# Performance work log

Measured on AMD Instinct MI355X. Metric: run time of the kernel, lower is better.

Reference implementation:

```python
import jax, jax.numpy as jnp
import numpy as np

MIN_NORM = 1e-15
BALL_EPS = 4e-3  # float32 boundary eps used by the PoincareBall manifold


def _norm(x):
    return jnp.maximum(jnp.linalg.norm(x, axis=-1, keepdims=True), MIN_NORM)


def _artanh(x):
    # clamp like torch Artanh autograd fn (1e-7 margin)
    return jnp.arctanh(jnp.clip(x, -1.0 + 1e-7, 1.0 - 1e-7))


def proj(x, c):
    n = _norm(x)
    maxnorm = (1.0 - BALL_EPS) / jnp.sqrt(c)
    return jnp.where(n > maxnorm, x / n * maxnorm, x)


def expmap0(u, c):
    sc = jnp.sqrt(c)
    n = _norm(u)
    return jnp.tanh(sc * n) * u / (sc * n)


def logmap0(p, c):
    sc = jnp.sqrt(c)
    n = _norm(p)
    return _artanh(sc * n) * p / (sc * n)


def mobius_add(x, y, c):
    x2 = jnp.sum(x * x, axis=-1, keepdims=True)
    y2 = jnp.sum(y * y, axis=-1, keepdims=True)
    xy = jnp.sum(x * y, axis=-1, keepdims=True)
    num = (1.0 + 2.0 * c * xy + c * y2) * x + (1.0 - c * x2) * y
    denom = 1.0 + 2.0 * c * xy + c * c * x2 * y2
    return num / jnp.maximum(denom, MIN_NORM)


def mobius_matvec(m, x, c):
    sc = jnp.sqrt(c)
    xn = _norm(x)
    mx = x @ m.T  # [N, out]
    mxn = _norm(mx)
    res = jnp.tanh(mxn / xn * _artanh(sc * xn)) * mx / (mxn * sc)
    is_zero = jnp.all(mx == 0, axis=-1, keepdims=True)
    return jnp.where(is_zero, jnp.zeros_like(res), res)


def setup_inputs() -> dict:
    key = jax.random.key(0)
    N, D_IN, D_OUT, E = 100000, 128, 128, 1600000
    k1, k2, k3, k4, k5 = jax.random.split(key, 5)
    # points inside the Poincare ball (||x|| ~ 0.34 < 1)
    x = 0.03 * jax.random.normal(k1, (N, D_IN), dtype=jnp.float32)
    # xavier_uniform with gain sqrt(2)
    limit = np.sqrt(2.0) * np.sqrt(6.0 / (D_IN + D_OUT))
    weight = jax.random.uniform(k2, (D_OUT, D_IN), minval=-limit, maxval=limit, dtype=jnp.float32)
    bias = jnp.zeros((D_OUT,), dtype=jnp.float32)
    edge_index = jax.random.randint(k3, (2, E), 0, N, dtype=jnp.int64)
    edge_weight = jax.random.uniform(k4, (E,), dtype=jnp.float32) / 16.0
    return {"x": x, "weight": weight, "bias": bias,
            "edge_index": edge_index, "edge_weight": edge_weight,
            "num_nodes": N}


def reference(x, weight, bias, edge_index, edge_weight, num_nodes):
    c_in = 1.0
    c_out = 1.0
    # --- OriginHypLinear (dropout=0 / eval) ---
    mv = proj(mobius_matvec(weight, x, c_in), c_in)
    hyp_bias = proj(expmap0(bias[None, :], c_in), c_in)  # proj_tan0 is identity
    h = proj(mobius_add(mv, hyp_bias, c_in), c_in)
    # --- OriginHypAgg: logmap0 -> spmm -> expmap0 ---
    xt = logmap0(h, c_in)
    dst, src = edge_index[0], edge_index[1]
    support = jax.ops.segment_sum(edge_weight[:, None] * xt[src], dst,
                                  num_segments=num_nodes)
    h = proj(expmap0(support, c_in), c_in)
    # --- OriginHypAct: relu in tangent space ---
    xt = jax.nn.relu(logmap0(h, c_in))  # proj_tan0 identity
    return proj(expmap0(xt, c_out), c_out)
```

## Files before the change

kernel.cpp:

```cpp
#include <hip/hip_runtime.h>
#include <math.h>

#define D 128
#define MAXNORM 0.996f
#define MINNORM 1e-15f
#define ATCLAMP (1.0f - 1e-7f)

#define CHUNK 2048
#define BSH   7
#define MAXNB 1024
#define SCAP2 5120
#define CAP   4096
#define TCAP  (1 << 20)

typedef unsigned int   u32;
typedef unsigned short u16;

typedef __attribute__((ext_vector_type(8))) _Float16 f16x8;
typedef __attribute__((ext_vector_type(2))) __fp16   h2raw;
typedef __attribute__((ext_vector_type(4))) float f32x4;

__device__ __forceinline__ float wsum(float v) {
#pragma unroll
  for (int m = 32; m; m >>= 1) v += __shfl_xor(v, m);
  return v;
}
__device__ __forceinline__ float rsum16(float v) {
#pragma unroll
  for (int m = 1; m <= 8; m <<= 1) v += __shfl_xor(v, m);
  return v;
}

__device__ __forceinline__ float frcp(float x) { return __builtin_amdgcn_rcpf(x); }

__device__ __forceinline__ float fast_artanh(float x) {
  x = fminf(x, ATCLAMP);
  return 0.5f * __logf((1.0f + x) * frcp(1.0f - x));
}
__device__ __forceinline__ float fast_tanh(float z) {
  float t = __expf(-2.0f * z);
  return (1.0f - t) * frcp(1.0f + t);
}

__device__ __forceinline__ float bflo(u32 u) { return __uint_as_float(u << 16); }
__device__ __forceinline__ float bfhi(u32 u) { return __uint_as_float(u & 0xffff0000u); }
__device__ __forceinline__ float bf2f(u16 h) { return __uint_as_float(((u32)h) << 16); }

union H2U { h2raw h; u32 u; };
__device__ __forceinline__ u32 pkh(float a, float b) {
  H2U c; c.h = __builtin_amdgcn_cvt_pkrtz(a, b); return c.u;
}
union U2H { u32 u; _Float16 h[2]; };
union U4H8 { uint4 u; f16x8 h; };
__device__ __forceinline__ f16x8 as_h8(uint4 v) { U4H8 c; c.u = v; return c.h; }
__device__ __forceinline__ u16 f2h(float f) {
  _Float16 h = (_Float16)f; return *(u16*)&h;
}

__device__ __forceinline__ bool detect_bf16(const u32* p) {
  float lo = fabsf(bflo(p[threadIdx.x & 63]));
  return (bool)__all(lo < 1.0f);
}
__device__ __forceinline__ bool detect_i64(const int* p) {
  return (bool)__all(p[2 * (threadIdx.x & 63) + 1] == 0);
}

template<bool BF>
__device__ __forceinline__ void k1_body(const void* xv, const void* Wv,
                                        const void* bv, u16* xt, int N,
                                        uint4* Wh) {
  const int tid  = threadIdx.x;
  const int lane = tid & 63;
  const int wid  = tid >> 6;
  const int qg   = lane >> 4;
  const int lc   = lane & 15;

  for (int slot = tid; slot < 2048; slot += 256) {
    const int l = slot & 63, frag = slot >> 6;
    const int t = frag >> 2, ks = frag & 3;
    const int j  = (l & 15) + 16 * t;
    const int k0 = 32 * ks + 8 * (l >> 4);
    float f[8];
    if (BF) {
      uint4 v = ((const uint4*)Wv)[j * 16 + (k0 >> 3)];
      f[0] = bflo(v.x); f[1] = bfhi(v.x); f[2] = bflo(v.y); f[3] = bfhi(v.y);
      f[4] = bflo(v.z); f[5] = bfhi(v.z); f[6] = bflo(v.w); f[7] = bfhi(v.w);
    } else {
      const float* Wf = (const float*)Wv;
      float4 f0 = *(const float4*)(Wf + (size_t)j * D + k0);
      float4 f1 = *(const float4*)(Wf + (size_t)j * D + k0 + 4);
      f[0]=f0.x; f[1]=f0.y; f[2]=f0.z; f[3]=f0.w;
      f[4]=f1.x; f[5]=f1.y; f[6]=f1.z; f[7]=f1.w;
    }
    Wh[slot] = make_uint4(pkh(f[0],f[1]), pkh(f[2],f[3]),
                          pkh(f[4],f[5]), pkh(f[6],f[7]));
  }

  float bfr[8];
  float nb2 = 0.f;
#pragma unroll
  for (int t = 0; t < 8; ++t) {
    float v = BF ? bf2f(((const u16*)bv)[lc + 16 * t])
                 : ((const float*)bv)[lc + 16 * t];
    bfr[t] = v; nb2 += v * v;
  }
  nb2 = rsum16(nb2);
  float y2;
  {
    float nb = fmaxf(sqrtf(nb2), MINNORM);
    float s  = fast_tanh(nb) * frcp(nb);
    float n1 = s * nb;
    if (n1 > MAXNORM) s *= MAXNORM * frcp(n1);
#pragma unroll
    for (int t = 0; t < 8; ++t) bfr[t] *= s;
    y2 = s * s * nb2;
  }
  const bool bias_zero = (y2 == 0.0f);

  __syncthreads();

  const int T = (N + 15) >> 4;
  const int tile = blockIdx.x * 4 + wid;
  if (tile >= T) return;
  {
    const int rbase = tile * 16;
    int rowA = rbase + lc; if (rowA >= N) rowA = N - 1;
    uint4 Ah[4];
    float xn2 = 0.f;
#pragma unroll
    for (int ks = 0; ks < 4; ++ks) {
      float f[8];
      if (BF) {
        uint4 v = ((const uint4*)((const u16*)xv + (size_t)rowA * D))[4 * ks + qg];
        f[0]=bflo(v.x); f[1]=bfhi(v.x); f[2]=bflo(v.y); f[3]=bfhi(v.y);
        f[4]=bflo(v.z); f[5]=bfhi(v.z); f[6]=bflo(v.w); f[7]=bfhi(v.w);
      } else {
        const float4* xr = (const float4*)((const float*)xv + (size_t)rowA * D);
        float4 f0 = xr[8 * ks + 2 * qg], f1 = xr[8 * ks + 2 * qg + 1];
        f[0]=f0.x; f[1]=f0.y; f[2]=f0.z; f[3]=f0.w;
        f[4]=f1.x; f[5]=f1.y; f[6]=f1.z; f[7]=f1.w;
      }
#pragma unroll
      for (int i = 0; i < 8; ++i) xn2 += f[i] * f[i];
      Ah[ks] = make_uint4(pkh(f[0],f[1]), pkh(f[2],f[3]),
                          pkh(f[4],f[5]), pkh(f[6],f[7]));
    }
    xn2 += __shfl_xor(xn2, 16);
    xn2 += __shfl_xor(xn2, 32);

    f32x4 acc[8];
    const f32x4 zero = {0.f, 0.f, 0.f, 0.f};
#pragma unroll
    for (int t = 0; t < 8; ++t) acc[t] = zero;
#pragma unroll
    for (int ks = 0; ks < 4; ++ks) {
      f16x8 a = as_h8(Ah[ks]);
#pragma unroll
      for (int t = 0; t < 8; ++t) {
        f16x8 bh = as_h8(Wh[(t * 4 + ks) * 64 + lane]);
        acc[t] = __builtin_amdgcn_mfma_f32_16x16x32_f16(a, bh, acc[t], 0, 0, 0);
      }
    }

#pragma unroll
    for (int q = 0; q < 4; ++q) {
      const int row_off = qg * 4 + q;
      const int row = rbase + row_off;
      float xnq = fmaxf(sqrtf(__shfl(xn2, row_off)), MINNORM);
      float s2 = 0.f;
#pragma unroll
      for (int t = 0; t < 8; ++t) { float v = acc[t][q]; s2 += v * v; }
      s2 = rsum16(s2);
      float mxn = fmaxf(sqrtf(s2), MINNORM);
      float r = fast_tanh(mxn * frcp(xnq) * fast_artanh(xnq)) * frcp(mxn);
      float pn = r * mxn;
      if (pn > MAXNORM) { r *= MAXNORM * frcp(pn); pn = MAXNORM; }
      float h[8];
      float hn;
      if (bias_zero) {
#pragma unroll
        for (int t = 0; t < 8; ++t) h[t] = r * acc[t][q];
        hn = pn;
      } else {
        float xy = 0.f;
#pragma unroll
        for (int t = 0; t < 8; ++t) { h[t] = r * acc[t][q]; xy += h[t] * bfr[t]; }
        xy = rsum16(xy);
        float x2 = pn * pn;
        float ca = 1.f + 2.f * xy + y2;
        float cb = 1.f - x2;
        float id = frcp(fmaxf(1.f + 2.f * xy + x2 * y2, MINNORM));
        float s3 = 0.f;
#pragma unroll
        for (int t = 0; t < 8; ++t) { h[t] = (ca * h[t] + cb * bfr[t]) * id; s3 += h[t] * h[t]; }
        hn = fmaxf(sqrtf(rsum16(s3)), MINNORM);
      }
      float ps = (hn > MAXNORM) ? (MAXNORM * frcp(hn)) : 1.f;
      float np = fmaxf(hn * ps, MINNORM);
      float tsc = fast_artanh(np) * frcp(np) * ps;
      if (row < N) {
        uint4 pk;
        pk.x = (u32)f2h(tsc * h[0]) | ((u32)f2h(tsc * h[1]) << 16);
        pk.y = (u32)f2h(tsc * h[2]) | ((u32)f2h(tsc * h[3]) << 16);
        pk.z = (u32)f2h(tsc * h[4]) | ((u32)f2h(tsc * h[5]) << 16);
        pk.w = (u32)f2h(tsc * h[6]) | ((u32)f2h(tsc * h[7]) << 16);
        *(uint4*)(xt + (size_t)row * D + lc * 8) = pk;
      }
    }
  }
}

__device__ __forceinline__ void ksA_body(
    const int* ei, const void* ew, uint2* ebuck, u16* soffs,
    int E, int N, int nb, int chunk, uint4* lds) {
  uint2* recs = (uint2*)lds;
  int*   hist = (int*)(lds + 1024);
  int*   sArr = hist + MAXNB;
  int*   psum = sArr + MAXNB + 1;
  const bool i64 = detect_i64(ei);
  const bool bf  = detect_bf16((const u32*)ew);
  const int tid   = threadIdx.x;
  const int cbase = chunk * CHUNK;

  for (int i = tid; i < MAXNB; i += 256) hist[i] = 0;
  __syncthreads();

  int bkt[8], rank[8]; u32 px[8], wb[8]; bool val[8];
#pragma unroll
  for (int r = 0; r < 8; ++r) {
    const int e = cbase + r * 256 + tid;
    val[r] = false;
    if (e < E) {
      int dst, src;
      if (i64) {
        dst = (int)((const uint2*)ei)[(size_t)e].x;
        src = (int)((const uint2*)ei)[(size_t)E + e].x;
      } else {
        dst = ei[e]; src = ei[(size_t)E + e];
      }
      if ((unsigned)dst < (unsigned)N && (unsigned)src < (unsigned)N) {
        val[r] = true;
        bkt[r] = dst >> BSH;
        px[r]  = (u32)src | ((u32)(dst & ((1 << BSH) - 1)) << 17);
        float w;
        if (bf) w = bf2f(((const u16*)ew)[e]); else w = ((const float*)ew)[e];
        wb[r] = __float_as_uint(w);
        rank[r] = atomicAdd(&hist[bkt[r]], 1);
      }
    }
  }
  __syncthreads();

  const int g0 = tid * 4;
  int loc[4], ts = 0;
#pragma unroll
  for (int i = 0; i < 4; ++i) { loc[i] = ts; ts += hist[g0 + i]; }
  psum[tid] = ts; __syncthreads();
#pragma unroll
  for (int off = 1; off < 256; off <<= 1) {
    int t = (tid >= off) ? psum[tid - off] : 0;
    __syncthreads();
    psum[tid] += t;
    __syncthreads();
  }
  const int excl = psum[tid] - ts;
#pragma unroll
  for (int i = 0; i < 4; ++i) sArr[g0 + i] = excl + loc[i];
  if (tid == 255) sArr[MAXNB] = psum[255];
  __syncthreads();

#pragma unroll
  for (int r = 0; r < 8; ++r) if (val[r])
    recs[sArr[bkt[r]] + rank[r]] = make_uint2(px[r], wb[r]);
  __syncthreads();

  const int vcnt = sArr[MAXNB];
  for (int i = tid; i < vcnt; i += 256) ebuck[(size_t)cbase + i] = recs[i];
  u16* so = soffs + (size_t)chunk * (nb + 1);
  for (int b = tid; b <= nb; b += 256) so[b] = (u16)sArr[b];
}

extern "C" __global__ __launch_bounds__(256)
void OriginHyperbolicGraphConvolution_38628935860614_kernel(
    const void* x, const void* W, const void* b, u16* xt,
    const int* ei, const void* ew, uint2* ebuck, u16* soffs, int* tailcur,
    int N, int E, int nb, int nk1) {
  __shared__ uint4 Wh[2048];
  if (blockIdx.x == 0 && threadIdx.x == 0) *tailcur = 0;
  if ((int)blockIdx.x < nk1) {
    if (detect_bf16((const u32*)x)) k1_body<true >(x, W, b, xt, N, Wh);
    else                            k1_body<false>(x, W, b, xt, N, Wh);
  } else {
    ksA_body(ei, ew, ebuck, soffs, E, N, nb, (int)blockIdx.x - nk1, Wh);
  }
}

extern "C" __global__ __launch_bounds__(256) void ks3(
    const uint2* ebuck, const u16* soffs, uint2* esrt, uint2* offs2,
    int* tailcur, int N, int nb, int nchunks) {
  __shared__ uint2 stage[SCAP2];
  __shared__ int red[256];
  __shared__ int hist[128], sc[128], cur[128];
  __shared__ int lcur;
  __shared__ u32 sbase;
  const int tid = threadIdx.x;
  const int b = blockIdx.x;
  const int node0 = b << BSH;

  int myc = 0;
  for (int c = tid; c < nchunks; c += 256) {
    const u16* so = soffs + (size_t)c * (nb + 1) + b;
    myc += (int)so[1] - (int)so[0];
  }
  red[tid] = myc;
  if (tid < 128) hist[tid] = 0;
  if (tid == 0) lcur = 0;
  __syncthreads();
#pragma unroll
  for (int off = 128; off; off >>= 1) {
    if (tid < off) red[tid] += red[tid + off];
    __syncthreads();
  }
  const int cnt = red[0];
  if (tid == 0)
    sbase = (cnt <= CAP) ? (u32)((size_t)b * CAP)
                         : (u32)((size_t)nb * CAP + (u32)atomicAdd(tailcur, cnt));
  __syncthreads();
  const u32 base = sbase;

  const bool fit = (cnt <= SCAP2);
  if (fit) {
    for (int c = tid; c < nchunks; c += 256) {
      const u16* so = soffs + (size_t)c * (nb + 1) + b;
      const int a = so[0], e = so[1];
      if (e > a) {
        const int sb = atomicAdd(&lcur, e - a);
        for (int j = a; j < e; ++j) {
          const uint2 r = ebuck[(size_t)c * CHUNK + j];
          stage[sb + (j - a)] = r;
          atomicAdd(&hist[(r.x >> 17) & 127], 1);
        }
      }
    }
  } else {
    for (int c = tid; c < nchunks; c += 256) {
      const u16* so = soffs + (size_t)c * (nb + 1) + b;
      for (int j = so[0]; j < so[1]; ++j)
        atomicAdd(&hist[(ebuck[(size_t)c * CHUNK + j].x >> 17) & 127], 1);
    }
  }
  __syncthreads();

  int v = 0;
  if (tid < 128) { v = hist[tid]; sc[tid] = v; }
  __syncthreads();
#pragma unroll
  for (int off = 1; off < 128; off <<= 1) {
    int t = (tid < 128 && tid >= off) ? sc[tid - off] : 0;
    __syncthreads();
    if (tid < 128) sc[tid] += t;
    __syncthreads();
  }
  if (tid < 128) {
    const int st = sc[tid] - v;
    cur[tid] = st;
    const int node = node0 + tid;
    if (node < N) offs2[node] = make_uint2(base + (u32)st, (u32)v);
  }
  __syncthreads();

  if (fit) {
    for (int i = tid; i < cnt; i += 256) {
      const uint2 r = stage[i];
      const int d = atomicAdd(&cur[(r.x >> 17) & 127], 1);
      esrt[(size_t)base + d] = make_uint2(r.x & 0x1FFFFu, r.y);
    }
  } else {
    for (int c = tid; c < nchunks; c += 256) {
      const u16* so = soffs + (size_t)c * (nb + 1) + b;
      for (int j = so[0]; j < so[1]; ++j) {
        const uint2 r = ebuck[(size_t)c * CHUNK + j];
        const int d = atomicAdd(&cur[(r.x >> 17) & 127], 1);
        esrt[(size_t)base + d] = make_uint2(r.x & 0x1FFFFu, r.y);
      }
    }
  }
}

extern "C" __global__ __launch_bounds__(256) void kagg(
    const uint2* offs2, const uint2* esrt, const u16* xt,
    void* out, const void* xdet, int N) {
  const bool bf = detect_bf16((const u32*)xdet);
  const int lane = threadIdx.x & 63;
  const int node = blockIdx.x * 4 + (threadIdx.x >> 6);
  if (node >= N) return;
  const uint2 oo = offs2[node];
  const int s0  = __builtin_amdgcn_readfirstlane((int)oo.x);
  const int cnt = __builtin_amdgcn_readfirstlane((int)oo.y);
  const uint2* ep = esrt + s0;
  const u32* xtw = (const u32*)xt;
  float a0 = 0.f, a1 = 0.f;
  int i = 0;
  for (; i + 16 <= cnt; i += 16) {
    uint2 e[16]; u32 u[16];
#pragma unroll
    for (int k = 0; k < 16; ++k) e[k] = ep[i + k];
#pragma unroll
    for (int k = 0; k < 16; ++k) u[k] = xtw[(e[k].x << 6) | lane];
#pragma unroll
    for (int k = 0; k < 16; ++k) {
      const float w = __uint_as_float(e[k].y);
      U2H c; c.u = u[k];
      a0 += w * (float)c.h[0];
      a1 += w * (float)c.h[1];
    }
  }
  for (; i + 4 <= cnt; i += 4) {
    uint2 e[4]; u32 u[4];
#pragma unroll
    for (int k = 0; k < 4; ++k) e[k] = ep[i + k];
#pragma unroll
    for (int k = 0; k < 4; ++k) u[k] = xtw[(e[k].x << 6) | lane];
#pragma unroll
    for (int k = 0; k < 4; ++k) {
      const float w = __uint_as_float(e[k].y);
      U2H c; c.u = u[k];
      a0 += w * (float)c.h[0];
      a1 += w * (float)c.h[1];
    }
  }
  for (; i < cnt; ++i) {
    const uint2 e = ep[i];
    const u32 u = xtw[(e.x << 6) | lane];
    const float w = __uint_as_float(e.y);
    U2H c; c.u = u;
    a0 += w * (float)c.h[0];
    a1 += w * (float)c.h[1];
  }
  float n = fmaxf(sqrtf(wsum(a0 * a0 + a1 * a1)), MINNORM);
  float tn = fast_tanh(n);
  float m = tn * frcp(n);
  if (tn > MAXNORM) { m *= MAXNORM * frcp(tn); tn = MAXNORM; }
  float nn = fmaxf(tn, MINNORM);
  m *= fast_artanh(nn) * frcp(nn);
  float tA = fmaxf(m * a0, 0.f), tB = fmaxf(m * a1, 0.f);
  float nr = fmaxf(sqrtf(wsum(tA * tA + tB * tB)), MINNORM);
  float t2 = fast_tanh(nr);
  float m2 = t2 * frcp(nr);
  if (t2 > MAXNORM) m2 *= MAXNORM * frcp(t2);
  float oA = m2 * tA, oB = m2 * tB;
  const int ls = (lane & 7) * 8 + (lane >> 4);
  const int el = (lane >> 3) & 1;
  const float A0 = __shfl(oA, ls),     B0 = __shfl(oB, ls);
  const float A1 = __shfl(oA, ls + 4), B1 = __shfl(oB, ls + 4);
  const float v0 = el ? B0 : A0;
  const float v1 = el ? B1 : A1;
  if (bf) {
    u32 ua = __float_as_uint(v0), ub = __float_as_uint(v1);
    u32 ra = (ua + 0x7fffu + ((ua >> 16) & 1u)) >> 16;
    u32 rb = (ub + 0x7fffu + ((ub >> 16) & 1u)) >> 16;
    ((u32*)out)[(size_t)node * 64 + lane] = ra | (rb << 16);
  } else {
    ((float2*)out)[(size_t)node * 64 + lane] = make_float2(v0, v1);
  }
}

extern "C" void kernel_launch(void* const* d_in, const int* in_sizes, int n_in,
                              void* d_out, int out_size, void* d_ws, size_t ws_size,
                              hipStream_t stream) {
  const void* x    = d_in[0];
  const void* W    = d_in[1];
  const void* bias = d_in[2];
  const int*  ei   = (const int*)d_in[3];
  const void* ew   = d_in[4];
  const int N = in_sizes[0] / D;
  const int E = in_sizes[4];
  const int nchunks = (E + CHUNK - 1) / CHUNK;
  const int nb      = (N + (1 << BSH) - 1) >> BSH;

  char* ws = (char*)d_ws;
  size_t off = 0;
  auto carve = [&](size_t bytes) { char* p = ws + off; off = (off + bytes + 255) & ~(size_t)255; return p; };
  u16*   xt    = (u16*)  carve((size_t)N * D * sizeof(u16));
  uint2* ebuck = (uint2*)carve((size_t)nchunks * CHUNK * sizeof(uint2));
  uint2* esrt  = (uint2*)carve(((size_t)nb * CAP + TCAP) * sizeof(uint2));
  u16*   soffs = (u16*)  carve((size_t)nchunks * (nb + 1) * sizeof(u16));
  uint2* offs2 = (uint2*)carve((size_t)N * sizeof(uint2));
  int*   tailcur = (int*)carve(256);

  const int T   = (N + 15) / 16;
  const int nk1 = (T + 3) / 4;

  OriginHyperbolicGraphConvolution_38628935860614_kernel<<<nk1 + nchunks, 256, 0, stream>>>(
      x, W, bias, xt, ei, ew, ebuck, soffs, tailcur, N, E, nb, nk1);
  ks3 <<<nb, 256, 0, stream>>>(ebuck, soffs, esrt, offs2, tailcur, N, nb, nchunks);
  kagg<<<(N + 3) / 4, 256, 0, stream>>>(offs2, esrt, xt, d_out, x, N);
}
```

Before: 253.1 us.

## Fuse bucket sort and aggregation into one kernel using shared-memory sorted edges

```diff
diff --git a/kernel.cpp b/kernel.cpp
--- a/kernel.cpp
+++ b/kernel.cpp
@@ -9,9 +9,7 @@
 #define CHUNK 2048
 #define BSH   7
 #define MAXNB 1024
-#define SCAP2 5120
-#define CAP   4096
-#define TCAP  (1 << 20)
+#define SCAP3 5120
 
 typedef unsigned int   u32;
 typedef unsigned short u16;
@@ -283,10 +281,9 @@
 extern "C" __global__ __launch_bounds__(256)
 void OriginHyperbolicGraphConvolution_38628935860614_kernel(
     const void* x, const void* W, const void* b, u16* xt,
-    const int* ei, const void* ew, uint2* ebuck, u16* soffs, int* tailcur,
+    const int* ei, const void* ew, uint2* ebuck, u16* soffs,
     int N, int E, int nb, int nk1) {
   __shared__ uint4 Wh[2048];
-  if (blockIdx.x == 0 && threadIdx.x == 0) *tailcur = 0;
   if ((int)blockIdx.x < nk1) {
     if (detect_bf16((const u32*)x)) k1_body<true >(x, W, b, xt, N, Wh);
     else                            k1_body<false>(x, W, b, xt, N, Wh);
@@ -295,148 +292,8 @@
   }
 }
 
-extern "C" __global__ __launch_bounds__(256) void ks3(
-    const uint2* ebuck, const u16* soffs, uint2* esrt, uint2* offs2,
-    int* tailcur, int N, int nb, int nchunks) {
-  __shared__ uint2 stage[SCAP2];
-  __shared__ int red[256];
-  __shared__ int hist[128], sc[128], cur[128];
-  __shared__ int lcur;
-  __shared__ u32 sbase;
-  const int tid = threadIdx.x;
-  const int b = blockIdx.x;
-  const int node0 = b << BSH;
-
-  int myc = 0;
-  for (int c = tid; c < nchunks; c += 256) {
-    const u16* so = soffs + (size_t)c * (nb + 1) + b;
-    myc += (int)so[1] - (int)so[0];
-  }
-  red[tid] = myc;
-  if (tid < 128) hist[tid] = 0;
-  if (tid == 0) lcur = 0;
-  __syncthreads();
-#pragma unroll
-  for (int off = 128; off; off >>= 1) {
-    if (tid < off) red[tid] += red[tid + off];
-    __syncthreads();
-  }
-  const int cnt = red[0];
-  if (tid == 0)
-    sbase = (cnt <= CAP) ? (u32)((size_t)b * CAP)
-                         : (u32)((size_t)nb * CAP + (u32)atomicAdd(tailcur, cnt));
-  __syncthreads();
-  const u32 base = sbase;
-
-  const bool fit = (cnt <= SCAP2);
-  if (fit) {
-    for (int c = tid; c < nchunks; c += 256) {
-      const u16* so = soffs + (size_t)c * (nb + 1) + b;
-      const int a = so[0], e = so[1];
-      if (e > a) {
-        const int sb = atomicAdd(&lcur, e - a);
-        for (int j = a; j < e; ++j) {
-          const uint2 r = ebuck[(size_t)c * CHUNK + j];
-          stage[sb + (j - a)] = r;
-          atomicAdd(&hist[(r.x >> 17) & 127], 1);
-        }
-      }
-    }
-  } else {
-    for (int c = tid; c < nchunks; c += 256) {
-      const u16* so = soffs + (size_t)c * (nb + 1) + b;
-      for (int j = so[0]; j < so[1]; ++j)
-        atomicAdd(&hist[(ebuck[(size_t)c * CHUNK + j].x >> 17) & 127], 1);
-    }
-  }
-  __syncthreads();
-
-  int v = 0;
-  if (tid < 128) { v = hist[tid]; sc[tid] = v; }
-  __syncthreads();
-#pragma unroll
-  for (int off = 1; off < 128; off <<= 1) {
-    int t = (tid < 128 && tid >= off) ? sc[tid - off] : 0;
-    __syncthreads();
-    if (tid < 128) sc[tid] += t;
-    __syncthreads();
-  }
-  if (tid < 128) {
-    const int st = sc[tid] - v;
-    cur[tid] = st;
-    const int node = node0 + tid;
-    if (node < N) offs2[node] = make_uint2(base + (u32)st, (u32)v);
-  }
-  __syncthreads();
-
-  if (fit) {
-    for (int i = tid; i < cnt; i += 256) {
-      const uint2 r = stage[i];
-      const int d = atomicAdd(&cur[(r.x >> 17) & 127], 1);
-      esrt[(size_t)base + d] = make_uint2(r.x & 0x1FFFFu, r.y);
-    }
-  } else {
-    for (int c = tid; c < nchunks; c += 256) {
-      const u16* so = soffs + (size_t)c * (nb + 1) + b;
-      for (int j = so[0]; j < so[1]; ++j) {
-        const uint2 r = ebuck[(size_t)c * CHUNK + j];
-        const int d = atomicAdd(&cur[(r.x >> 17) & 127], 1);
-        esrt[(size_t)base + d] = make_uint2(r.x & 0x1FFFFu, r.y);
-      }
-    }
-  }
-}
-
-extern "C" __global__ __launch_bounds__(256) void kagg(
-    const uint2* offs2, const uint2* esrt, const u16* xt,
-    void* out, const void* xdet, int N) {
-  const bool bf = detect_bf16((const u32*)xdet);
-  const int lane = threadIdx.x & 63;
-  const int node = blockIdx.x * 4 + (threadIdx.x >> 6);
-  if (node >= N) return;
-  const uint2 oo = offs2[node];
-  const int s0  = __builtin_amdgcn_readfirstlane((int)oo.x);
-  const int cnt = __builtin_amdgcn_readfirstlane((int)oo.y);
-  const uint2* ep = esrt + s0;
-  const u32* xtw = (const u32*)xt;
-  float a0 = 0.f, a1 = 0.f;
-  int i = 0;
-  for (; i + 16 <= cnt; i += 16) {
-    uint2 e[16]; u32 u[16];
-#pragma unroll
-    for (int k = 0; k < 16; ++k) e[k] = ep[i + k];
-#pragma unroll
-    for (int k = 0; k < 16; ++k) u[k] = xtw[(e[k].x << 6) | lane];
-#pragma unroll
-    for (int k = 0; k < 16; ++k) {
-      const float w = __uint_as_float(e[k].y);
-      U2H c; c.u = u[k];
-      a0 += w * (float)c.h[0];
-      a1 += w * (float)c.h[1];
-    }
-  }
-  for (; i + 4 <= cnt; i += 4) {
-    uint2 e[4]; u32 u[4];
-#pragma unroll
-    for (int k = 0; k < 4; ++k) e[k] = ep[i + k];
-#pragma unroll
-    for (int k = 0; k < 4; ++k) u[k] = xtw[(e[k].x << 6) | lane];
-#pragma unroll
-    for (int k = 0; k < 4; ++k) {
-      const float w = __uint_as_float(e[k].y);
-      U2H c; c.u = u[k];
-      a0 += w * (float)c.h[0];
-      a1 += w * (float)c.h[1];
-    }
-  }
-  for (; i < cnt; ++i) {
-    const uint2 e = ep[i];
-    const u32 u = xtw[(e.x << 6) | lane];
-    const float w = __uint_as_float(e.y);
-    U2H c; c.u = u;
-    a0 += w * (float)c.h[0];
-    a1 += w * (float)c.h[1];
-  }
+__device__ __forceinline__ void finalize_store(
+    float a0, float a1, int node, int lane, bool bf, void* out) {
   float n = fmaxf(sqrtf(wsum(a0 * a0 + a1 * a1)), MINNORM);
   float tn = fast_tanh(n);
   float m = tn * frcp(n);
@@ -465,6 +322,134 @@
   }
 }
 
+extern "C" __global__ __launch_bounds__(512) void kfin(
+    const uint2* ebuck, const u16* soffs, const u16* xt,
+    void* out, const void* xdet, int N, int nb, int nchunks) {
+  __shared__ uint2 srt[SCAP3];
+  __shared__ int hist[128], nstart[128], cur[128], sc[128];
+  __shared__ int redv[512];
+  const bool bf = detect_bf16((const u32*)xdet);
+  const int tid = threadIdx.x;
+  const int lane = tid & 63, wid = tid >> 6;
+  const int b = blockIdx.x;
+  const int node0 = b << BSH;
+  const u32* xtw = (const u32*)xt;
+
+  if (tid < 128) hist[tid] = 0;
+  __syncthreads();
+
+  int myc = 0;
+  for (int c = tid; c < nchunks; c += 512) {
+    const u16* so = soffs + (size_t)c * (nb + 1) + b;
+    const int a = so[0], e = so[1];
+    myc += e - a;
+    for (int j = a; j < e; ++j)
+      atomicAdd(&hist[(ebuck[(size_t)c * CHUNK + j].x >> 17) & 127], 1);
+  }
+  redv[tid] = myc;
+  __syncthreads();
+#pragma unroll
+  for (int off = 256; off; off >>= 1) {
+    if (tid < off) redv[tid] += redv[tid + off];
+    __syncthreads();
+  }
+  const int cnt = redv[0];
+
+  int v = 0;
+  if (tid < 128) { v = hist[tid]; sc[tid] = v; }
+  __syncthreads();
+#pragma unroll
+  for (int off = 1; off < 128; off <<= 1) {
+    int t = (tid < 128 && tid >= off) ? sc[tid - off] : 0;
+    __syncthreads();
+    if (tid < 128) sc[tid] += t;
+    __syncthreads();
+  }
+  if (tid < 128) { nstart[tid] = sc[tid] - v; cur[tid] = sc[tid] - v; }
+  __syncthreads();
+
+  if (cnt <= SCAP3) {
+    for (int c = tid; c < nchunks; c += 512) {
+      const u16* so = soffs + (size_t)c * (nb + 1) + b;
+      for (int j = so[0]; j < so[1]; ++j) {
+        const uint2 r = ebuck[(size_t)c * CHUNK + j];
+        const int d = atomicAdd(&cur[(r.x >> 17) & 127], 1);
+        srt[d] = make_uint2(r.x & 0x1FFFFu, r.y);
+      }
+    }
+    __syncthreads();
+
+    for (int k = 0; k < 16; ++k) {
+      const int nloc = wid + 8 * k;
+      const int node = node0 + nloc;
+      if (node >= N) continue;
+      const int s0 = nstart[nloc];
+      const int c2 = hist[nloc];
+      float a0 = 0.f, a1 = 0.f;
+      int i = 0;
+      for (; i + 16 <= c2; i += 16) {
+        uint2 e[16]; u32 u[16];
+#pragma unroll
+        for (int q = 0; q < 16; ++q) e[q] = srt[s0 + i + q];
+#pragma unroll
+        for (int q = 0; q < 16; ++q) u[q] = xtw[(e[q].x << 6) | lane];
+#pragma unroll
+        for (int q = 0; q < 16; ++q) {
+          const float w = __uint_as_float(e[q].y);
+          U2H c; c.u = u[q];
+          a0 += w * (float)c.h[0];
+          a1 += w * (float)c.h[1];
+        }
+      }
+      for (; i + 4 <= c2; i += 4) {
+        uint2 e[4]; u32 u[4];
+#pragma unroll
+        for (int q = 0; q < 4; ++q) e[q] = srt[s0 + i + q];
+#pragma unroll
+        for (int q = 0; q < 4; ++q) u[q] = xtw[(e[q].x << 6) | lane];
+#pragma unroll
+        for (int q = 0; q < 4; ++q) {
+          const float w = __uint_as_float(e[q].y);
+          U2H c; c.u = u[q];
+          a0 += w * (float)c.h[0];
+          a1 += w * (float)c.h[1];
+        }
+      }
+      for (; i < c2; ++i) {
+        const uint2 e = srt[s0 + i];
+        const u32 u = xtw[(e.x << 6) | lane];
+        const float w = __uint_as_float(e.y);
+        U2H c; c.u = u;
+        a0 += w * (float)c.h[0];
+        a1 += w * (float)c.h[1];
+      }
+      finalize_store(a0, a1, node, lane, bf, out);
+    }
+  } else {
+    for (int k = 0; k < 16; ++k) {
+      const int nloc = wid + 8 * k;
+      const int node = node0 + nloc;
+      if (node >= N) continue;
+      float a0 = 0.f, a1 = 0.f;
+      for (int c = 0; c < nchunks; ++c) {
+        const u16* so = soffs + (size_t)c * (nb + 1) + b;
+        const int a = so[0], e = so[1];
+        for (int j = a; j < e; ++j) {
+          const uint2 r = ebuck[(size_t)c * CHUNK + j];
+          if ((int)((r.x >> 17) & 127) == nloc) {
+            const u32 u = xtw[((r.x & 0x1FFFFu) << 6) | lane];
+            const float w = __uint_as_float(r.y);
+            U2H cc; cc.u = u;
+            a0 += w * (float)cc.h[0];
+            a1 += w * (float)cc.h[1];
+          }
+        }
+      }
+      finalize_store(a0, a1, node, lane, bf, out);
+    }
+  }
+}
+
 extern "C" void kernel_launch(void* const* d_in, const int* in_sizes, int n_in,
                               void* d_out, int out_size, void* d_ws, size_t ws_size,
                               hipStream_t stream) {
@@ -483,16 +468,12 @@
   auto carve = [&](size_t bytes) { char* p = ws + off; off = (off + bytes + 255) & ~(size_t)255; return p; };
   u16*   xt    = (u16*)  carve((size_t)N * D * sizeof(u16));
   uint2* ebuck = (uint2*)carve((size_t)nchunks * CHUNK * sizeof(uint2));
-  uint2* esrt  = (uint2*)carve(((size_t)nb * CAP + TCAP) * sizeof(uint2));
   u16*   soffs = (u16*)  carve((size_t)nchunks * (nb + 1) * sizeof(u16));
-  uint2* offs2 = (uint2*)carve((size_t)N * sizeof(uint2));
-  int*   tailcur = (int*)carve(256);
 
   const int T   = (N + 15) / 16;
   const int nk1 = (T + 3) / 4;
 
   OriginHyperbolicGraphConvolution_38628935860614_kernel<<<nk1 + nchunks, 256, 0, stream>>>(
-      x, W, bias, xt, ei, ew, ebuck, soffs, tailcur, N, E, nb, nk1);
-  ks3 <<<nb, 256, 0, stream>>>(ebuck, soffs, esrt, offs2, tailcur, N, nb, nchunks);
-  kagg<<<(N + 3) / 4, 256, 0, stream>>>(offs2, esrt, xt, d_out, x, N);
-}
+      x, W, bias, xt, ei, ew, ebuck, soffs, N, E, nb, nk1);
+  kfin<<<nb, 512, 0, stream>>>(ebuck, soffs, xt, d_out, x, N, nb, nchunks);
+}
```

Measured after the change: 276.4 us. +9.2%, slower.

## Split dense transform across first two launches to overlap with edge bucketing/sort

Applied to the files above, without the earlier changes.

```diff
diff --git a/kernel.cpp b/kernel.cpp
--- a/kernel.cpp
+++ b/kernel.cpp
@@ -68,7 +68,7 @@
 template<bool BF>
 __device__ __forceinline__ void k1_body(const void* xv, const void* Wv,
                                         const void* bv, u16* xt, int N,
-                                        uint4* Wh) {
+                                        uint4* Wh, int blk, int tbase) {
   const int tid  = threadIdx.x;
   const int lane = tid & 63;
   const int wid  = tid >> 6;
@@ -120,7 +120,7 @@
   __syncthreads();
 
   const int T = (N + 15) >> 4;
-  const int tile = blockIdx.x * 4 + wid;
+  const int tile = tbase + blk * 4 + wid;
   if (tile >= T) return;
   {
     const int rbase = tile * 16;
@@ -284,27 +284,30 @@
 void OriginHyperbolicGraphConvolution_38628935860614_kernel(
     const void* x, const void* W, const void* b, u16* xt,
     const int* ei, const void* ew, uint2* ebuck, u16* soffs, int* tailcur,
-    int N, int E, int nb, int nk1) {
+    int N, int E, int nb, int nchunks) {
   __shared__ uint4 Wh[2048];
   if (blockIdx.x == 0 && threadIdx.x == 0) *tailcur = 0;
-  if ((int)blockIdx.x < nk1) {
-    if (detect_bf16((const u32*)x)) k1_body<true >(x, W, b, xt, N, Wh);
-    else                            k1_body<false>(x, W, b, xt, N, Wh);
+  if ((int)blockIdx.x < nchunks) {
+    ksA_body(ei, ew, ebuck, soffs, E, N, nb, (int)blockIdx.x, Wh);
   } else {
-    ksA_body(ei, ew, ebuck, soffs, E, N, nb, (int)blockIdx.x - nk1, Wh);
-  }
-}
-
-extern "C" __global__ __launch_bounds__(256) void ks3(
+    if (detect_bf16((const u32*)x))
+      k1_body<true >(x, W, b, xt, N, Wh, (int)blockIdx.x - nchunks, 0);
+    else
+      k1_body<false>(x, W, b, xt, N, Wh, (int)blockIdx.x - nchunks, 0);
+  }
+}
+
+__device__ __forceinline__ void ks3_body(
     const uint2* ebuck, const u16* soffs, uint2* esrt, uint2* offs2,
-    int* tailcur, int N, int nb, int nchunks) {
-  __shared__ uint2 stage[SCAP2];
-  __shared__ int red[256];
-  __shared__ int hist[128], sc[128], cur[128];
-  __shared__ int lcur;
-  __shared__ u32 sbase;
+    int* tailcur, int N, int nb, int nchunks, int b, char* smem) {
+  uint2* stage = (uint2*)smem;
+  int*   red   = (int*)(smem + 40960);
+  int*   hist  = (int*)(smem + 41984);
+  int*   sc    = (int*)(smem + 42496);
+  int*   cur   = (int*)(smem + 43008);
+  int*   lcur  = (int*)(smem + 43520);
+  u32*   sbase = (u32*)(smem + 43524);
   const int tid = threadIdx.x;
-  const int b = blockIdx.x;
   const int node0 = b << BSH;
 
   int myc = 0;
@@ -314,7 +317,7 @@
   }
   red[tid] = myc;
   if (tid < 128) hist[tid] = 0;
-  if (tid == 0) lcur = 0;
+  if (tid == 0) *lcur = 0;
   __syncthreads();
 #pragma unroll
   for (int off = 128; off; off >>= 1) {
@@ -323,10 +326,10 @@
   }
   const int cnt = red[0];
   if (tid == 0)
-    sbase = (cnt <= CAP) ? (u32)((size_t)b * CAP)
-                         : (u32)((size_t)nb * CAP + (u32)atomicAdd(tailcur, cnt));
-  __syncthreads();
-  const u32 base = sbase;
+    *sbase = (cnt <= CAP) ? (u32)((size_t)b * CAP)
+                          : (u32)((size_t)nb * CAP + (u32)atomicAdd(tailcur, cnt));
+  __syncthreads();
+  const u32 base = *sbase;
 
   const bool fit = (cnt <= SCAP2);
   if (fit) {
@@ -334,7 +337,7 @@
       const u16* so = soffs + (size_t)c * (nb + 1) + b;
       const int a = so[0], e = so[1];
       if (e > a) {
-        const int sb = atomicAdd(&lcur, e - a);
+        const int sb = atomicAdd(lcur, e - a);
         for (int j = a; j < e; ++j) {
           const uint2 r = ebuck[(size_t)c * CHUNK + j];
           stage[sb + (j - a)] = r;
@@ -384,6 +387,22 @@
         esrt[(size_t)base + d] = make_uint2(r.x & 0x1FFFFu, r.y);
       }
     }
+  }
+}
+
+extern "C" __global__ __launch_bounds__(256) void kB(
+    const void* x, const void* W, const void* b, u16* xt,
+    const uint2* ebuck, const u16* soffs, uint2* esrt, uint2* offs2,
+    int* tailcur, int N, int nb, int nchunks, int tbase) {
+  __shared__ uint4 smem[2721];
+  if ((int)blockIdx.x < nb) {
+    ks3_body(ebuck, soffs, esrt, offs2, tailcur, N, nb, nchunks,
+             (int)blockIdx.x, (char*)smem);
+  } else {
+    if (detect_bf16((const u32*)x))
+      k1_body<true >(x, W, b, xt, N, smem, (int)blockIdx.x - nb, tbase);
+    else
+      k1_body<false>(x, W, b, xt, N, smem, (int)blockIdx.x - nb, tbase);
   }
 }
 
@@ -488,11 +507,14 @@
   uint2* offs2 = (uint2*)carve((size_t)N * sizeof(uint2));
   int*   tailcur = (int*)carve(256);
 
-  const int T   = (N + 15) / 16;
-  const int nk1 = (T + 3) / 4;
-
-  OriginHyperbolicGraphConvolution_38628935860614_kernel<<<nk1 + nchunks, 256, 0, stream>>>(
-      x, W, bias, xt, ei, ew, ebuck, soffs, tailcur, N, E, nb, nk1);
-  ks3 <<<nb, 256, 0, stream>>>(ebuck, soffs, esrt, offs2, tailcur, N, nb, nchunks);
+  const int T    = (N + 15) / 16;
+  const int nk1  = (T + 3) / 4;
+  const int nk1a = nk1 / 2;
+  const int nk1b = nk1 - nk1a;
+
+  OriginHyperbolicGraphConvolution_38628935860614_kernel<<<nchunks + nk1a, 256, 0, stream>>>(
+      x, W, bias, xt, ei, ew, ebuck, soffs, tailcur, N, E, nb, nchunks);
+  kB<<<nb + nk1b, 256, 0, stream>>>(
+      x, W, bias, xt, ebuck, soffs, esrt, offs2, tailcur, N, nb, nchunks, nk1a * 4);
   kagg<<<(N + 3) / 4, 256, 0, stream>>>(offs2, esrt, xt, d_out, x, N);
 }
```

Measured after the change: 245.1 us. -3.2%, faster.
